# Performance work log

Hardware: AMD Instinct MI355X
Metric: run time of the kernel (lower is better)

## Reference

```python
import jax, jax.numpy as jnp
import numpy as np

PADDING = 1

def setup_inputs() -> dict:
    key = jax.random.key(0)
    k1, k2 = jax.random.split(key)
    imgs = jax.random.normal(k1, (8, 32, 32, 32), dtype=jnp.float32)
    kernel = jax.random.normal(k2, (32, 32, 3, 3), dtype=jnp.float32)
    return {"imgs": imgs, "kernel": kernel}

def reference(imgs, kernel):
    # Tropical max-plus 'convolution' (kind='conv': kernel spatially flipped),
    # groups=1, stride=1, dilation=1, padding=PADDING with semifield zero = -inf.
    B, C, H, W = imgs.shape
    O, Ck, kh, kw = kernel.shape
    OY = H + 2 * PADDING - (kh - 1)
    OX = W + 2 * PADDING - (kw - 1)
    neg_inf = jnp.array(-jnp.inf, dtype=imgs.dtype)
    x = jnp.pad(imgs, ((0, 0), (0, 0), (PADDING, PADDING), (PADDING, PADDING)),
                constant_values=neg_inf)
    # conv flips the kernel spatially
    k = kernel[:, :, ::-1, ::-1]
    # im2col windows: [B, C, kh*kw, OY, OX] (small fixed loop over kernel taps)
    windows = jnp.stack(
        [x[:, :, dy:dy + OY, dx:dx + OX] for dy in range(kh) for dx in range(kw)],
        axis=2,
    )
    # broadcast 'multiply' (tropical: add): [B, O, C, kh*kw, OY, OX]
    mult = windows[:, None] + k.reshape(1, O, C, kh * kw, 1, 1)
    # tropical add-reduce (max) over channels and kernel taps
    out = jnp.max(mult, axis=(2, 3))  # [B, O, OY, OX]
    return out
```

## Files before the change

kernel.cpp:

```cpp
#include <hip/hip_runtime.h>
#include <math.h>


constexpr int B = 8, C = 32, O = 32, H = 32, W = 32;
constexpr int LW = 40;
constexpr int ROWS = 10;

__global__ __launch_bounds__(256, 2) void trop_conv_kernel(
    const float* __restrict__ img, const float* __restrict__ kern,
    float* __restrict__ out) {
  __shared__ float simg[C][ROWS][LW];

  const int tid = threadIdx.x;
  const int blk = blockIdx.x;
  const int rowgrp = blk & 3;
  const int o0 = ((blk >> 2) & 15) * 2;
  const int b = blk >> 6;
  const int y0 = rowgrp * 8 - 1;

  const float4* img4 = (const float4*)(img + b * C * H * W);
  float4* simg4 = (float4*)simg;
  for (int i = tid; i < C * ROWS * (LW / 4); i += 256) {
    int seg = i % (LW / 4);
    int cr = i / (LW / 4);
    int r = cr % ROWS;
    int c = cr / ROWS;
    int gy = y0 + r;
    float4 v = make_float4(-INFINITY, -INFINITY, -INFINITY, -INFINITY);
    if (seg >= 1 && seg <= 8 && gy >= 0 && gy < H) {
      v = img4[(c * H + gy) * (W / 4) + (seg - 1)];
    }
    simg4[i] = v;
  }
  __syncthreads();

  const int x = tid & 31;
  const int ylocal = tid >> 5;

  const float* wA = kern + (size_t)(o0 + 0) * C * 9;
  const float* wB = kern + (size_t)(o0 + 1) * C * 9;

  float a0 = -INFINITY, a1 = -INFINITY, a2 = -INFINITY;
  float b0 = -INFINITY, b1 = -INFINITY, b2 = -INFINITY;

#pragma unroll
  for (int c = 0; c < C; ++c) {
    const float* srow = &simg[c][ylocal][x + 3];
#pragma unroll
    for (int dy = 0; dy < 3; ++dy) {
      float v0 = srow[dy * LW + 0];
      float v1 = srow[dy * LW + 1];
      float v2 = srow[dy * LW + 2];
      int wb = c * 9 + (2 - dy) * 3;
      float tA = fmaxf(fmaxf(v0 + wA[wb + 2], v1 + wA[wb + 1]), v2 + wA[wb + 0]);
      float tB = fmaxf(fmaxf(v0 + wB[wb + 2], v1 + wB[wb + 1]), v2 + wB[wb + 0]);
      if (dy == 0) { a0 = fmaxf(a0, tA); b0 = fmaxf(b0, tB); }
      else if (dy == 1) { a1 = fmaxf(a1, tA); b1 = fmaxf(b1, tB); }
      else { a2 = fmaxf(a2, tA); b2 = fmaxf(b2, tB); }
    }
  }

  const int y = rowgrp * 8 + ylocal;
  float* op = out + (((size_t)b * O + o0) * H + y) * W + x;
  op[0] = fmaxf(fmaxf(a0, a1), a2);
  op[H * W] = fmaxf(fmaxf(b0, b1), b2);
}

extern "C" void kernel_launch(void* const* d_in, const int* in_sizes, int n_in,
                              void* d_out, int out_size, void* d_ws, size_t ws_size,
                              hipStream_t stream) {
  const float* img = (const float*)d_in[0];
  const float* kern = (const float*)d_in[1];
  float* out = (float*)d_out;
  trop_conv_kernel<<<dim3(B * (O / 2) * 4), dim3(256), 0, stream>>>(img, kern, out);
}
```

Measured before the change: 72.17 us.

## Register-tile two output rows per thread, use lane shuffles for horizontal neighbors

Drops the shared-memory staging of a padded image tile. Each thread now reads four image rows per channel straight from global memory and gets the left and right neighbors through wavefront shuffles, with explicit masking at the borders. Each thread computes a 2x2 block of outputs (two rows by two output channels), so every loaded row feeds more outputs. Weights move into shared memory with a 16-float stride so they can be read as float4. The block shrinks to 128 threads, which lowers parallelism per block and relies on L1/L2 caching to absorb the repeated global image reads.

```diff
diff --git a/kernel.cpp b/kernel.cpp
--- a/kernel.cpp
+++ b/kernel.cpp
@@ -3,67 +3,113 @@
 
 
 constexpr int B = 8, C = 32, O = 32, H = 32, W = 32;
-constexpr int LW = 40;
-constexpr int ROWS = 10;
 
-__global__ __launch_bounds__(256, 2) void trop_conv_kernel(
+__device__ __forceinline__ float f3(float a, float b, float c) {
+  return fmaxf(fmaxf(a, b), c);
+}
+
+__global__ __launch_bounds__(128, 2) void trop_conv_kernel(
     const float* __restrict__ img, const float* __restrict__ kern,
     float* __restrict__ out) {
-  __shared__ float simg[C][ROWS][LW];
+  __shared__ float sw[2 * 32 * 16];
 
   const int tid = threadIdx.x;
   const int blk = blockIdx.x;
-  const int rowgrp = blk & 3;
-  const int o0 = ((blk >> 2) & 15) * 2;
+  const int yq = blk & 3;
+  const int op = (blk >> 2) & 15;
   const int b = blk >> 6;
-  const int y0 = rowgrp * 8 - 1;
 
-  const float4* img4 = (const float4*)(img + b * C * H * W);
-  float4* simg4 = (float4*)simg;
-  for (int i = tid; i < C * ROWS * (LW / 4); i += 256) {
-    int seg = i % (LW / 4);
-    int cr = i / (LW / 4);
-    int r = cr % ROWS;
-    int c = cr / ROWS;
-    int gy = y0 + r;
-    float4 v = make_float4(-INFINITY, -INFINITY, -INFINITY, -INFINITY);
-    if (seg >= 1 && seg <= 8 && gy >= 0 && gy < H) {
-      v = img4[(c * H + gy) * (W / 4) + (seg - 1)];
-    }
-    simg4[i] = v;
+  const float* kw = kern + op * 576;
+  for (int j = tid; j < 576; j += 128) {
+    int po = j >= 288;
+    int r = j - po * 288;
+    int c = r / 9;
+    int t = r - c * 9;
+    sw[po * 512 + c * 16 + t] = kw[j];
   }
   __syncthreads();
 
   const int x = tid & 31;
-  const int ylocal = tid >> 5;
+  const int ytl = tid >> 5;
+  const int y0 = yq * 8 + ytl * 2;
 
-  const float* wA = kern + (size_t)(o0 + 0) * C * 9;
-  const float* wB = kern + (size_t)(o0 + 1) * C * 9;
+  int ro0, ro1, ro2, ro3;
+  {
+    int yy0 = y0 - 1; yy0 = yy0 < 0 ? 0 : yy0;
+    int yy3 = y0 + 2; yy3 = yy3 > 31 ? 31 : yy3;
+    ro0 = yy0 * W + x;
+    ro1 = y0 * W + x;
+    ro2 = (y0 + 1) * W + x;
+    ro3 = yy3 * W + x;
+  }
+  const bool top_oob = (y0 == 0);
+  const bool bot_oob = (y0 == 30);
+  const bool xz = (x == 0);
+  const bool xe = (x == 31);
+  const float NEG = -__builtin_huge_valf();
 
-  float a0 = -INFINITY, a1 = -INFINITY, a2 = -INFINITY;
-  float b0 = -INFINITY, b1 = -INFINITY, b2 = -INFINITY;
+  const float* ib = img + b * C * H * W;
 
-#pragma unroll
+  float a00 = NEG, a10 = NEG;
+  float a01 = NEG, a11 = NEG;
+
+#pragma unroll 8
   for (int c = 0; c < C; ++c) {
-    const float* srow = &simg[c][ylocal][x + 3];
-#pragma unroll
-    for (int dy = 0; dy < 3; ++dy) {
-      float v0 = srow[dy * LW + 0];
-      float v1 = srow[dy * LW + 1];
-      float v2 = srow[dy * LW + 2];
-      int wb = c * 9 + (2 - dy) * 3;
-      float tA = fmaxf(fmaxf(v0 + wA[wb + 2], v1 + wA[wb + 1]), v2 + wA[wb + 0]);
-      float tB = fmaxf(fmaxf(v0 + wB[wb + 2], v1 + wB[wb + 1]), v2 + wB[wb + 0]);
-      if (dy == 0) { a0 = fmaxf(a0, tA); b0 = fmaxf(b0, tB); }
-      else if (dy == 1) { a1 = fmaxf(a1, tA); b1 = fmaxf(b1, tB); }
-      else { a2 = fmaxf(a2, tA); b2 = fmaxf(b2, tB); }
+    const float* ic = ib + c * H * W;
+    float v0 = ic[ro0];
+    float v1 = ic[ro1];
+    float v2 = ic[ro2];
+    float v3 = ic[ro3];
+    v0 = top_oob ? NEG : v0;
+    v3 = bot_oob ? NEG : v3;
+
+    float l0 = __shfl_up(v0, 1), r0 = __shfl_down(v0, 1);
+    float l1 = __shfl_up(v1, 1), r1 = __shfl_down(v1, 1);
+    float l2 = __shfl_up(v2, 1), r2 = __shfl_down(v2, 1);
+    float l3 = __shfl_up(v3, 1), r3 = __shfl_down(v3, 1);
+    l0 = xz ? NEG : l0;  r0 = xe ? NEG : r0;
+    l1 = xz ? NEG : l1;  r1 = xe ? NEG : r1;
+    l2 = xz ? NEG : l2;  r2 = xe ? NEG : r2;
+    l3 = xz ? NEG : l3;  r3 = xe ? NEG : r3;
+
+    const float4 A0 = *(const float4*)&sw[c * 16];
+    const float4 A1 = *(const float4*)&sw[c * 16 + 4];
+    const float A8 = sw[c * 16 + 8];
+    const float4 B0 = *(const float4*)&sw[512 + c * 16];
+    const float4 B1 = *(const float4*)&sw[512 + c * 16 + 4];
+    const float B8 = sw[512 + c * 16 + 8];
+
+    {
+      float t0 = f3(l0 + A8, v0 + A1.w, r0 + A1.z);
+      float t1 = f3(l1 + A1.y, v1 + A1.x, r1 + A0.w);
+      float t2 = f3(l2 + A0.z, v2 + A0.y, r2 + A0.x);
+      a00 = fmaxf(a00, f3(t0, t1, t2));
+    }
+    {
+      float t0 = f3(l1 + A8, v1 + A1.w, r1 + A1.z);
+      float t1 = f3(l2 + A1.y, v2 + A1.x, r2 + A0.w);
+      float t2 = f3(l3 + A0.z, v3 + A0.y, r3 + A0.x);
+      a10 = fmaxf(a10, f3(t0, t1, t2));
+    }
+    {
+      float t0 = f3(l0 + B8, v0 + B1.w, r0 + B1.z);
+      float t1 = f3(l1 + B1.y, v1 + B1.x, r1 + B0.w);
+      float t2 = f3(l2 + B0.z, v2 + B0.y, r2 + B0.x);
+      a01 = fmaxf(a01, f3(t0, t1, t2));
+    }
+    {
+      float t0 = f3(l1 + B8, v1 + B1.w, r1 + B1.z);
+      float t1 = f3(l2 + B1.y, v2 + B1.x, r2 + B0.w);
+      float t2 = f3(l3 + B0.z, v3 + B0.y, r3 + B0.x);
+      a11 = fmaxf(a11, f3(t0, t1, t2));
     }
   }
 
-  const int y = rowgrp * 8 + ylocal;
-  float* op = out + (((size_t)b * O + o0) * H + y) * W + x;
-  op[0] = fmaxf(fmaxf(a0, a1), a2);
-  op[H * W] = fmaxf(fmaxf(b0, b1), b2);
+  const int o0 = op * 2;
+  out[((b * O + o0) * H + y0) * W + x] = a00;
+  out[((b * O + o0) * H + y0 + 1) * W + x] = a10;
+  out[((b * O + o0 + 1) * H + y0) * W + x] = a01;
+  out[((b * O + o0 + 1) * H + y0 + 1) * W + x] = a11;
 }
 
 extern "C" void kernel_launch(void* const* d_in, const int* in_sizes, int n_in,
@@ -72,5 +118,5 @@
   const float* img = (const float*)d_in[0];
   const float* kern = (const float*)d_in[1];
   float* out = (float*)d_out;
-  trop_conv_kernel<<<dim3(B * (O / 2) * 4), dim3(256), 0, stream>>>(img, kern, out);
+  trop_conv_kernel<<<dim3(512), dim3(128), 0, stream>>>(img, kern, out);
 }
```

Measured after the change: 71.97 us. No clear change (-0.3%).
